# Optimization experiments

Hardware: AMD Instinct MI355X
Metric: run time of the kernel (lower is better)

## Reference

```python
import jax, jax.numpy as jnp
import numpy as np
from jax import lax

NUM_CODEBOOKS = 8
CODEBOOK_SIZE = 1024
HIDDEN_DIM = 512
NUM_LAYERS = 4
KSIZE = 15
COMMIT = 0.25


def _conv1d(x, w, b, stride, pad):
    # x: [B, Cin, L], w: [Cout, Cin, K] (torch Conv1d layout == OIH)
    y = lax.conv_general_dilated(x, w, window_strides=(stride,), padding=[(pad, pad)],
                                 dimension_numbers=('NCH', 'OIH', 'NCH'))
    return y + b[None, :, None]


def _conv_transpose1d(x, w, b):
    # torch ConvTranspose1d(k=15, stride=2, padding=7, output_padding=1)
    # w: [Cin, Cout, K] (torch layout). Equivalent fwd conv: flip kernel, swap io,
    # lhs_dilation=stride, padding=(K-1-pad, K-1-pad+output_padding) = (7, 8).
    wf = jnp.flip(w, -1).transpose(1, 0, 2)  # [Cout, Cin, K]
    y = lax.conv_general_dilated(x, wf, window_strides=(1,), padding=[(7, 8)],
                                 lhs_dilation=(2,), dimension_numbers=('NCH', 'OIH', 'NCH'))
    return y + b[None, :, None]


def _vq(residual, cb):
    # residual: [B, D, T], cb: [K, D]
    B, D, T = residual.shape
    z = residual.transpose(0, 2, 1).reshape(-1, D)  # [B*T, D]
    # ||z||^2 - 2 z C^T + ||C||^2
    dists = (z * z).sum(1, keepdims=True) - 2.0 * (z @ cb.T) + (cb * cb).sum(1)
    codes = jnp.argmin(dists, axis=1)  # [B*T]
    z_q = cb[codes].reshape(B, T, D).transpose(0, 2, 1)  # [B, D, T]
    commitment = jnp.mean((lax.stop_gradient(z_q) - residual) ** 2)
    codebook_l = jnp.mean((z_q - lax.stop_gradient(residual)) ** 2)
    vq_loss = codebook_l + COMMIT * commitment
    z_q_st = residual + lax.stop_gradient(z_q - residual)  # straight-through
    return z_q_st, vq_loss, codes.reshape(-1)


def _codec_forward(audio, enc_ws, enc_bs, codebooks, dec_ws, dec_bs):
    # encoder
    x = audio
    for w, b in zip(enc_ws, enc_bs):
        x = jax.nn.elu(_conv1d(x, w, b, stride=2, pad=7))
    z = x  # [B, 512, T]
    # residual VQ
    quantized = jnp.zeros_like(z)
    residual = z
    total_loss = jnp.float32(0.0)
    all_codes = []
    for i in range(NUM_CODEBOOKS):
        z_q, vq_loss, codes = _vq(residual, codebooks[i])
        quantized = quantized + z_q
        residual = residual - z_q
        total_loss = total_loss + vq_loss
        all_codes.append(codes)
    # decoder
    y = quantized
    for w, b in zip(dec_ws[:-1], dec_bs[:-1]):
        y = jax.nn.elu(_conv_transpose1d(y, w, b))
    y = jnp.tanh(_conv_transpose1d(y, dec_ws[-1], dec_bs[-1]))
    return y, total_loss, all_codes


def setup_inputs() -> dict:
    key = jax.random.key(0)
    ks = jax.random.split(key, 32)
    B, S = 8, 65536
    audio = jax.random.normal(ks[0], (B, 1, S), dtype=jnp.float32)
    # encoder channels: 1 -> 64 -> 128 -> 256 -> 512
    enc_ch = [1, 64, 128, 256, 512]
    inp = {'audio': audio}
    for i in range(NUM_LAYERS):
        cin, cout = enc_ch[i], enc_ch[i + 1]
        fan = cin * KSIZE
        inp[f'enc_w{i}'] = jax.random.normal(ks[1 + i], (cout, cin, KSIZE), jnp.float32) / np.sqrt(fan)
        inp[f'enc_b{i}'] = jnp.zeros((cout,), jnp.float32)
    # codebooks ~ U(-1/K, 1/K)
    inp['codebooks'] = jax.random.uniform(ks[10], (NUM_CODEBOOKS, CODEBOOK_SIZE, HIDDEN_DIM),
                                          jnp.float32, -1.0 / CODEBOOK_SIZE, 1.0 / CODEBOOK_SIZE)
    # decoder (torch ConvTranspose layout [Cin, Cout, K]): 512->256->128->64->1
    dec_ch = [512, 256, 128, 64, 1]
    for i in range(NUM_LAYERS):
        cin, cout = dec_ch[i], dec_ch[i + 1]
        fan = cin * KSIZE
        inp[f'dec_w{i}'] = jax.random.normal(ks[20 + i], (cin, cout, KSIZE), jnp.float32) / np.sqrt(fan)
        inp[f'dec_b{i}'] = jnp.zeros((cout,), jnp.float32)
    return inp


def reference(audio, enc_w0, enc_b0, enc_w1, enc_b1, enc_w2, enc_b2, enc_w3, enc_b3,
              codebooks, dec_w0, dec_b0, dec_w1, dec_b1, dec_w2, dec_b2, dec_w3, dec_b3):
    enc_ws = [enc_w0, enc_w1, enc_w2, enc_w3]
    enc_bs = [enc_b0, enc_b1, enc_b2, enc_b3]
    dec_ws = [dec_w0, dec_w1, dec_w2, dec_w3]
    dec_bs = [dec_b0, dec_b1, dec_b2, dec_b3]
    recon, vq_loss, codes = _codec_forward(audio, enc_ws, enc_bs, codebooks, dec_ws, dec_bs)
    return (recon, vq_loss, *codes)
```

## Files before the change

kernel.cpp:

```cpp
#include <hip/hip_runtime.h>
#include <hip/hip_bf16.h>
#include <math.h>

#define NCB 8
#define CBS 1024
#define HID 512
#define NB 8
#define TLAT 4096
#define DELTA 6.0e-5f

__global__ void rd_sentinel(float* out, float v)
{
    out[threadIdx.x] = v;
}

template<int CIN, int COUT, int LIN>
__global__ __launch_bounds__(256)
void rd_enc(const float* __restrict__ x, const float* __restrict__ w,
            const float* __restrict__ bias, float* __restrict__ y)
{
    constexpr int LOUT = LIN / 2;
    __shared__ float xs[2][528];
    const int tid = threadIdx.x;
    const int t0  = blockIdx.x * 512;
    const int t   = t0 + tid * 2;
    const int co0 = blockIdx.y * 4;
    const int b   = blockIdx.z;
    const float* xb = x + (size_t)b * CIN * LIN;
    const int base = 2 * t0 - 8;

    double acc[4][2];
#pragma unroll
    for (int c = 0; c < 4; ++c) acc[c][0] = acc[c][1] = (double)bias[co0 + c];

    for (int ci = 0; ci < CIN; ++ci) {
        const float* xc = xb + (size_t)ci * LIN;
        __syncthreads();
        for (int j = tid; j < 1040; j += 256) {
            const int xi = base + j;
            xs[j & 1][j >> 1] = ((unsigned)xi < (unsigned)LIN) ? xc[xi] : 0.f;
        }
        __syncthreads();
        const float* wc = w + ((size_t)co0 * CIN + ci) * 15;
#pragma unroll
        for (int k = 0; k < 15; ++k) {
            const int p = (k + 1) & 1;
            const int j = 2 * tid + ((k + 1) >> 1);
            const double x0 = (double)xs[p][j];
            const double x1 = (double)xs[p][j + 1];
#pragma unroll
            for (int c = 0; c < 4; ++c) {
                const double wv = (double)wc[c * CIN * 15 + k];
                acc[c][0] = fma(wv, x0, acc[c][0]);
                acc[c][1] = fma(wv, x1, acc[c][1]);
            }
        }
    }
#pragma unroll
    for (int c = 0; c < 4; ++c) {
        float* yp = y + ((size_t)b * COUT + co0 + c) * LOUT + t;
        const double a0 = acc[c][0], a1 = acc[c][1];
        yp[0] = (float)(a0 > 0.0 ? a0 : expm1(a0));
        yp[1] = (float)(a1 > 0.0 ? a1 : expm1(a1));
    }
}

template<int CIN, int COUT, int LIN, int CO_PER, int ACT>
__global__ __launch_bounds__(256)
void rd_dec(const float* __restrict__ x, const float* __restrict__ w,
            const float* __restrict__ bias, float* __restrict__ y)
{
    constexpr int LOUT = LIN * 2;
    const int u   = blockIdx.x * 256 + threadIdx.x;
    const int co0 = blockIdx.y * CO_PER;
    const int b   = blockIdx.z;

    float acc[CO_PER][2];
#pragma unroll
    for (int c = 0; c < CO_PER; ++c) acc[c][0] = acc[c][1] = bias[co0 + c];

    const float* xb = x + (size_t)b * CIN * LIN;
    for (int ci = 0; ci < CIN; ++ci) {
        const float* xc = xb + (size_t)ci * LIN;
        const float* wc = w + ((size_t)ci * COUT + co0) * 15;
#pragma unroll
        for (int dj = 0; dj < 8; ++dj) {
            const int j = u - 3 + dj;
            const float xv = ((unsigned)j < (unsigned)LIN) ? xc[j] : 0.f;
            const int ke = 13 - 2 * dj;
            const int ko = 14 - 2 * dj;
#pragma unroll
            for (int c = 0; c < CO_PER; ++c) {
                if (ke >= 0) acc[c][0] = fmaf(xv, wc[c * 15 + ke], acc[c][0]);
                acc[c][1] = fmaf(xv, wc[c * 15 + ko], acc[c][1]);
            }
        }
    }
#pragma unroll
    for (int c = 0; c < CO_PER; ++c) {
        float* yp = y + ((size_t)b * COUT + co0 + c) * LOUT + 2 * (size_t)u;
        if (ACT == 0) {
            yp[0] = acc[c][0] > 0.f ? acc[c][0] : expm1f(acc[c][0]);
            yp[1] = acc[c][1] > 0.f ? acc[c][1] : expm1f(acc[c][1]);
        } else {
            yp[0] = tanhf(acc[c][0]);
            yp[1] = tanhf(acc[c][1]);
        }
    }
}

__global__ __launch_bounds__(64)
void rd_prep(const float* __restrict__ cb, float* __restrict__ cnormF,
             float* __restrict__ lossp)
{
    __shared__ double red[64];
    const int rrow = blockIdx.x;
    const float* src = cb + (size_t)rrow * HID;
    const int lane = threadIdx.x;
    double s = 0.0;
#pragma unroll
    for (int m = 0; m < 8; ++m) {
        const float v = src[lane * 8 + m];
        s += (double)__fmul_rn(v, v);
    }
    red[lane] = s;
    __syncthreads();
    if (lane == 0) {
        double tot = 0.0;
        for (int i = 0; i < 64; ++i) tot += red[i];
        cnormF[rrow] = (float)tot;
        if (rrow == 0) lossp[0] = 0.f;
    }
}

__global__ __launch_bounds__(256)
void rd_z(const float* __restrict__ R, float* __restrict__ Zrow)
{
    __shared__ double zp[64][4];
    const int tid = threadIdx.x;
    const int gr0 = blockIdx.x * 64;
    const int b = gr0 >> 12, t0 = gr0 & 4095;
    const float* Rb = R + (size_t)b * HID * TLAT + t0;
    const int row = tid & 63, p = tid >> 6;
    double s = 0.0;
    const int d0 = p * 128;
    for (int d = d0; d < d0 + 128; ++d) {
        const float v = Rb[(size_t)d * TLAT + row];
        s += (double)__fmul_rn(v, v);
    }
    zp[row][p] = s;
    __syncthreads();
    if (tid < 64)
        Zrow[gr0 + tid] = (float)(((zp[tid][0] + zp[tid][1]) + zp[tid][2]) + zp[tid][3]);
}

__global__ __launch_bounds__(256)
void rd_pref(const float* __restrict__ cb, const float* __restrict__ cnormF,
             const float* __restrict__ R, float* __restrict__ tileMin)
{
    __shared__ __align__(16) float Rt[32][64];
    __shared__ __align__(16) float Ct[32][128];
    const int tid = threadIdx.x;
    const int gr0 = blockIdx.x * 64;
    const int cb0 = blockIdx.y * 128;
    const int b = gr0 >> 12, t0 = gr0 & 4095;
    const float* Rb = R + (size_t)b * HID * TLAT + t0;
    const int ir = tid >> 4, jc = tid & 15;

    float acc[4][8];
#pragma unroll
    for (int r = 0; r < 4; ++r)
#pragma unroll
        for (int c = 0; c < 8; ++c) acc[r][c] = 0.f;

    for (int kc = 0; kc < 16; ++kc) {
        const int k0 = kc * 32;
        __syncthreads();
#pragma unroll
        for (int l = 0; l < 8; ++l) {
            const int e = l * 256 + tid;
            Rt[e >> 6][e & 63] = Rb[(size_t)(k0 + (e >> 6)) * TLAT + (e & 63)];
        }
        {
            const int cc = tid >> 1, h = (tid & 1) * 16;
            const float* s = cb + (size_t)(cb0 + cc) * HID + k0 + h;
            const float4 v0 = *(const float4*)s;
            const float4 v1 = *(const float4*)(s + 4);
            const float4 v2 = *(const float4*)(s + 8);
            const float4 v3 = *(const float4*)(s + 12);
            Ct[h + 0][cc] = v0.x; Ct[h + 1][cc] = v0.y; Ct[h + 2][cc] = v0.z; Ct[h + 3][cc] = v0.w;
            Ct[h + 4][cc] = v1.x; Ct[h + 5][cc] = v1.y; Ct[h + 6][cc] = v1.z; Ct[h + 7][cc] = v1.w;
            Ct[h + 8][cc] = v2.x; Ct[h + 9][cc] = v2.y; Ct[h +10][cc] = v2.z; Ct[h +11][cc] = v2.w;
            Ct[h +12][cc] = v3.x; Ct[h +13][cc] = v3.y; Ct[h +14][cc] = v3.z; Ct[h +15][cc] = v3.w;
        }
        __syncthreads();

#pragma unroll
        for (int kk = 0; kk < 32; ++kk) {
            const float4 rv = *(const float4*)&Rt[kk][ir * 4];
            const float4 c0v = *(const float4*)&Ct[kk][jc * 8];
            const float4 c1v = *(const float4*)&Ct[kk][jc * 8 + 4];
            const float rr[4] = {rv.x, rv.y, rv.z, rv.w};
            const float cc8[8] = {c0v.x, c0v.y, c0v.z, c0v.w, c1v.x, c1v.y, c1v.z, c1v.w};
#pragma unroll
            for (int r = 0; r < 4; ++r)
#pragma unroll
                for (int c = 0; c < 8; ++c)
                    acc[r][c] = fmaf(rr[r], cc8[c], acc[r][c]);
        }
    }

#pragma unroll
    for (int r = 0; r < 4; ++r) {
        float m = 3.0e38f;
#pragma unroll
        for (int c = 0; c < 8; ++c) {
            const int ci = cb0 + jc * 8 + c;
            const float s = fmaf(-2.f, acc[r][c], cnormF[ci]);
            m = fminf(m, s);
        }
        const float o = __shfl_xor(m, 1, 64);
        m = fminf(m, o);
        if ((jc & 1) == 0)
            tileMin[(size_t)(gr0 + ir * 4 + r) * 64 + (cb0 >> 4) + (jc >> 1)] = m;
    }
}

__global__ __launch_bounds__(256)
void rd_fin(const float* __restrict__ cb, const float* __restrict__ cnormF,
            const float* __restrict__ R, const float* __restrict__ Zrow,
            const float* __restrict__ tileMin, unsigned short* __restrict__ codesOut)
{
    __shared__ float pm[64][4];
    __shared__ float rowMinS[64];
    __shared__ unsigned char tlist[64][16];
    __shared__ int tcnt[64];
    __shared__ int maxcS;
    __shared__ float bvS[64][4];
    __shared__ int   bcS[64][4];

    const int tid = threadIdx.x;
    const int gr0 = blockIdx.x * 64;
    const int b = gr0 >> 12, t0 = gr0 & 4095;
    const float* Rb = R + (size_t)b * HID * TLAT + t0;
    const int row = tid & 63, p = tid >> 6;
    const float* tmr = tileMin + (size_t)(gr0 + row) * 64;

    float m = 3.0e38f;
    for (int j = 0; j < 16; ++j) m = fminf(m, tmr[p * 16 + j]);
    pm[row][p] = m;
    if (tid == 0) maxcS = 0;
    __syncthreads();
    if (tid < 64)
        rowMinS[tid] = fminf(fminf(pm[tid][0], pm[tid][1]), fminf(pm[tid][2], pm[tid][3]));
    __syncthreads();

    if (tid < 64) {
        int cnt = 0;
        const float thr_ = rowMinS[tid] + DELTA;
        const float* tr = tileMin + (size_t)(gr0 + tid) * 64;
        for (int tt = 0; tt < 64; ++tt)
            if (tr[tt] <= thr_) { if (cnt < 16) tlist[tid][cnt] = (unsigned char)tt; ++cnt; }
        if (cnt > 16) cnt = 64;
        tcnt[tid] = cnt;
        atomicMax(&maxcS, cnt);
    }
    __syncthreads();
    const int maxc = maxcS;
    const int myCnt = tcnt[row];
    const float Zr = Zrow[gr0 + row];

    float bestS = 3.0e38f; int bestC = 0x7fffffff;
    for (int li = 0; li < maxc; ++li) {
        int tt = -1;
        if (li < myCnt) tt = (myCnt <= 16) ? (int)tlist[row][li] : li;
        if (tt >= 0) {
            const float* cp = cb + (size_t)(tt * 16 + p * 4) * HID;
            double a0 = 0.0, a1 = 0.0, a2 = 0.0, a3 = 0.0;
            for (int d = 0; d < 512; ++d) {
                const double rv = (double)Rb[(size_t)d * TLAT + row];
                a0 = fma(rv, (double)cp[d],        a0);
                a1 = fma(rv, (double)cp[d + 512],  a1);
                a2 = fma(rv, (double)cp[d + 1024], a2);
                a3 = fma(rv, (double)cp[d + 1536], a3);
            }
            const double aa[4] = {a0, a1, a2, a3};
#pragma unroll
            for (int c = 0; c < 4; ++c) {
                const int ci = tt * 16 + p * 4 + c;
                const float M32 = (float)aa[c];
                const float s = __fadd_rn(__fsub_rn(Zr, __fadd_rn(M32, M32)), cnormF[ci]);
                if (s < bestS || (s == bestS && ci < bestC)) { bestS = s; bestC = ci; }
            }
        }
    }
    bvS[row][p] = bestS; bcS[row][p] = bestC;
    __syncthreads();
    if (tid < 64) {
        float mv = 3.0e38f; int mc = 0x7fffffff;
#pragma unroll
        for (int q = 0; q < 4; ++q) {
            const float v = bvS[tid][q]; const int c = bcS[tid][q];
            if (v < mv || (v == mv && c < mc)) { mv = v; mc = c; }
        }
        codesOut[gr0 + tid] = (unsigned short)mc;
    }
}

__global__ __launch_bounds__(256)
void rd_comb(const float* __restrict__ cb, const unsigned short* __restrict__ codesIn,
             float* __restrict__ R, float* __restrict__ Q,
             float* __restrict__ loss_acc, int stage)
{
    __shared__ int codes_l[64];
    const int tid = threadIdx.x;
    const int gr0 = blockIdx.x * 64;
    const int b = gr0 >> 12, t0 = gr0 & 4095;
    float* Rb = R + (size_t)b * HID * TLAT + t0;
    float* Qb = Q + (size_t)b * HID * TLAT + t0;

    if (tid < 64) codes_l[tid] = (int)codesIn[gr0 + tid];
    __syncthreads();

    float ls = 0.f;
    for (int e = tid; e < 64 * HID; e += 256) {
        const int row = e & 63, d = e >> 6;
        const size_t off = (size_t)d * TLAT + row;
        const float rr = Rb[off];
        const int c = codes_l[row];
        const float q = cb[(size_t)c * HID + d];
        const float diff  = __fsub_rn(q, rr);
        const float zqst  = __fadd_rn(rr, diff);
        ls = fmaf(diff, diff, ls);
        Rb[off] = __fsub_rn(rr, zqst);
        if (stage == 0) Qb[off] = zqst; else Qb[off] = __fadd_rn(Qb[off], zqst);
    }
#pragma unroll
    for (int off = 32; off; off >>= 1) ls += __shfl_down(ls, off, 64);
    if ((tid & 63) == 0) atomicAdd(loss_acc, ls);
}

__global__ __launch_bounds__(256)
void rd_emit(const float* __restrict__ reconF, const unsigned short* __restrict__ codes_ws,
             const float* __restrict__ loss_acc, float* __restrict__ out)
{
    const int j = blockIdx.x * 256 + threadIdx.x;
    if (j >= 524288 + 1 + NCB * 32768) return;
    if (j < 524288)       out[j] = reconF[j];
    else if (j == 524288) out[j] = loss_acc[0] * 1.25f * (1.0f / 16777216.0f);
    else                  out[j] = (float)codes_ws[j - 524289];
}

extern "C" void kernel_launch(void* const* d_in, const int* in_sizes, int n_in,
                              void* d_out, int out_size, void* d_ws, size_t ws_size,
                              hipStream_t stream)
{
    float* out = (float*)d_out;

    if (n_in != 18)                                   { rd_sentinel<<<1, 256, 0, stream>>>(out, 1111.0f); return; }
    if (in_sizes[0] != 8 * 65536 || in_sizes[9] != NCB * CBS * HID ||
        in_sizes[1] != 64 * 15 || in_sizes[10] != 512 * 256 * 15)
                                                      { rd_sentinel<<<1, 256, 0, stream>>>(out, 3333.0f); return; }
    if (out_size != 524288 + 1 + NCB * 32768)         { rd_sentinel<<<1, 256, 0, stream>>>(out, 5555.0f); return; }
    if (ws_size < (size_t)137 * 1024 * 1024)          { rd_sentinel<<<1, 256, 0, stream>>>(out, 7777.0f); return; }

    const float* audio = (const float*)d_in[0];
    const float *ew[4], *eb[4], *dw[4], *db[4];
    for (int i = 0; i < 4; ++i) { ew[i] = (const float*)d_in[1 + 2 * i]; eb[i] = (const float*)d_in[2 + 2 * i]; }
    const float* cbs = (const float*)d_in[9];
    for (int i = 0; i < 4; ++i) { dw[i] = (const float*)d_in[10 + 2 * i]; db[i] = (const float*)d_in[11 + 2 * i]; }

    char* ws = (char*)d_ws;
    float*  A        = (float*)ws;
    float*  Bb       = (float*)(ws + (size_t)64 * 1024 * 1024);
    float*  tileMin  = (float*)(ws + (size_t)128 * 1024 * 1024);
    float*  reconF   = (float*)(ws + (size_t)128 * 1024 * 1024);
    unsigned short* codes_ws = (unsigned short*)(ws + (size_t)136 * 1024 * 1024);
    float*  cnormF   = (float*)(ws + (size_t)136 * 1024 * 1024 + 524288);
    float*  Zrow     = (float*)(ws + (size_t)136 * 1024 * 1024 + 524288 + 32768);
    float*  lossp    = (float*)(ws + (size_t)136 * 1024 * 1024 + 524288 + 32768 + 131072);

    rd_prep<<<NCB * CBS, 64, 0, stream>>>(cbs, cnormF, lossp);

    rd_enc<1,   64,  65536><<<dim3(64, 16,  NB), 256, 0, stream>>>(audio, ew[0], eb[0], A);
    rd_enc<64,  128, 32768><<<dim3(32, 32,  NB), 256, 0, stream>>>(A,  ew[1], eb[1], Bb);
    rd_enc<128, 256, 16384><<<dim3(16, 64,  NB), 256, 0, stream>>>(Bb, ew[2], eb[2], A);
    rd_enc<256, 512, 8192 ><<<dim3(8,  128, NB), 256, 0, stream>>>(A,  ew[3], eb[3], Bb);

    for (int i = 0; i < NCB; ++i) {
        const float* cbi = cbs + (size_t)i * CBS * HID;
        const float* cni = cnormF + (size_t)i * CBS;
        rd_z   <<<512, 256, 0, stream>>>(Bb, Zrow);
        rd_pref<<<dim3(512, 8), 256, 0, stream>>>(cbi, cni, Bb, tileMin);
        rd_fin <<<512, 256, 0, stream>>>(cbi, cni, Bb, Zrow, tileMin,
                                         codes_ws + (size_t)i * 32768);
        rd_comb<<<512, 256, 0, stream>>>(cbi, codes_ws + (size_t)i * 32768,
                                         Bb, A, lossp, i);
    }

    rd_dec<512, 256, 4096,  4, 0><<<dim3(16,  64, NB), 256, 0, stream>>>(A,  dw[0], db[0], Bb);
    rd_dec<256, 128, 8192,  4, 0><<<dim3(32,  32, NB), 256, 0, stream>>>(Bb, dw[1], db[1], A);
    rd_dec<128, 64,  16384, 4, 0><<<dim3(64,  16, NB), 256, 0, stream>>>(A,  dw[2], db[2], Bb);
    rd_dec<64,  1,   32768, 1, 1><<<dim3(128, 1,  NB), 256, 0, stream>>>(Bb, dw[3], db[3], reconF);

    rd_emit<<<3073, 256, 0, stream>>>(reconF, codes_ws, lossp, out);
}
```

Before: 18.58 ms.

## Transpose latent to row-major for VQ stage and remap encoder output pairs

Adds a tiled transpose kernel that converts the encoder output from [B, D, T] to [B*T, D] before the residual VQ loop and back afterwards. The VQ kernels (norms, distance tiles, refinement, combine) now read and write contiguous rows with vectorised float4 loads instead of strided column accesses. The encoder conv also changes each thread's two outputs from adjacent to 256 apart, giving coalesced stores and conflict-free LDS reads. The cost is two extra full-tensor transposes.

New measurement: 19.08 ms. +2.7%, slower.

```diff
diff --git a/kernel.cpp b/kernel.cpp
--- a/kernel.cpp
+++ b/kernel.cpp
@@ -9,21 +9,20 @@
 #define TLAT 4096
 #define DELTA 6.0e-5f
 
-__global__ void rd_sentinel(float* out, float v)
+__global__ void re_sentinel(float* out, float v)
 {
     out[threadIdx.x] = v;
 }
 
 template<int CIN, int COUT, int LIN>
 __global__ __launch_bounds__(256)
-void rd_enc(const float* __restrict__ x, const float* __restrict__ w,
+void re_enc(const float* __restrict__ x, const float* __restrict__ w,
             const float* __restrict__ bias, float* __restrict__ y)
 {
     constexpr int LOUT = LIN / 2;
-    __shared__ float xs[2][528];
+    __shared__ float xs[2][520];
     const int tid = threadIdx.x;
     const int t0  = blockIdx.x * 512;
-    const int t   = t0 + tid * 2;
     const int co0 = blockIdx.y * 4;
     const int b   = blockIdx.z;
     const float* xb = x + (size_t)b * CIN * LIN;
@@ -36,18 +35,18 @@
     for (int ci = 0; ci < CIN; ++ci) {
         const float* xc = xb + (size_t)ci * LIN;
         __syncthreads();
-        for (int j = tid; j < 1040; j += 256) {
-            const int xi = base + j;
-            xs[j & 1][j >> 1] = ((unsigned)xi < (unsigned)LIN) ? xc[xi] : 0.f;
+        for (int idx = tid; idx < 1040; idx += 256) {
+            const int xi = base + idx;
+            xs[idx & 1][idx >> 1] = ((unsigned)xi < (unsigned)LIN) ? xc[xi] : 0.f;
         }
         __syncthreads();
         const float* wc = w + ((size_t)co0 * CIN + ci) * 15;
 #pragma unroll
         for (int k = 0; k < 15; ++k) {
-            const int p = (k + 1) & 1;
-            const int j = 2 * tid + ((k + 1) >> 1);
-            const double x0 = (double)xs[p][j];
-            const double x1 = (double)xs[p][j + 1];
+            const int p  = (k + 1) & 1;
+            const int jb = (k + 1) >> 1;
+            const double x0 = (double)xs[p][tid + jb];
+            const double x1 = (double)xs[p][tid + 256 + jb];
 #pragma unroll
             for (int c = 0; c < 4; ++c) {
                 const double wv = (double)wc[c * CIN * 15 + k];
@@ -58,16 +57,34 @@
     }
 #pragma unroll
     for (int c = 0; c < 4; ++c) {
-        float* yp = y + ((size_t)b * COUT + co0 + c) * LOUT + t;
+        float* yp = y + ((size_t)b * COUT + co0 + c) * LOUT;
         const double a0 = acc[c][0], a1 = acc[c][1];
-        yp[0] = (float)(a0 > 0.0 ? a0 : expm1(a0));
-        yp[1] = (float)(a1 > 0.0 ? a1 : expm1(a1));
-    }
+        yp[t0 + tid]       = (float)(a0 > 0.0 ? a0 : expm1(a0));
+        yp[t0 + tid + 256] = (float)(a1 > 0.0 ? a1 : expm1(a1));
+    }
+}
+
+template<int RIN, int CIN_>
+__global__ __launch_bounds__(256)
+void re_tr(const float* __restrict__ in, float* __restrict__ out)
+{
+    __shared__ float tile[32][33];
+    const int c0 = blockIdx.x * 32, r0 = blockIdx.y * 32, b = blockIdx.z;
+    const int lx = threadIdx.x & 31, ly = threadIdx.x >> 5;
+    const float* ib = in + (size_t)b * RIN * CIN_;
+    float* ob = out + (size_t)b * RIN * CIN_;
+#pragma unroll
+    for (int m = 0; m < 4; ++m)
+        tile[ly + m * 8][lx] = ib[(size_t)(r0 + ly + m * 8) * CIN_ + c0 + lx];
+    __syncthreads();
+#pragma unroll
+    for (int m = 0; m < 4; ++m)
+        ob[(size_t)(c0 + ly + m * 8) * RIN + r0 + lx] = tile[lx][ly + m * 8];
 }
 
 template<int CIN, int COUT, int LIN, int CO_PER, int ACT>
 __global__ __launch_bounds__(256)
-void rd_dec(const float* __restrict__ x, const float* __restrict__ w,
+void re_dec(const float* __restrict__ x, const float* __restrict__ w,
             const float* __restrict__ bias, float* __restrict__ y)
 {
     constexpr int LOUT = LIN * 2;
@@ -110,7 +127,7 @@
 }
 
 __global__ __launch_bounds__(64)
-void rd_prep(const float* __restrict__ cb, float* __restrict__ cnormF,
+void re_prep(const float* __restrict__ cb, float* __restrict__ cnormF,
              float* __restrict__ lossp)
 {
     __shared__ double red[64];
@@ -134,18 +151,16 @@
 }
 
 __global__ __launch_bounds__(256)
-void rd_z(const float* __restrict__ R, float* __restrict__ Zrow)
+void re_z(const float* __restrict__ R, float* __restrict__ Zrow)
 {
     __shared__ double zp[64][4];
     const int tid = threadIdx.x;
     const int gr0 = blockIdx.x * 64;
-    const int b = gr0 >> 12, t0 = gr0 & 4095;
-    const float* Rb = R + (size_t)b * HID * TLAT + t0;
     const int row = tid & 63, p = tid >> 6;
+    const float* Rr = R + (size_t)(gr0 + row) * HID + p * 128;
     double s = 0.0;
-    const int d0 = p * 128;
-    for (int d = d0; d < d0 + 128; ++d) {
-        const float v = Rb[(size_t)d * TLAT + row];
+    for (int i = 0; i < 128; ++i) {
+        const float v = Rr[i];
         s += (double)__fmul_rn(v, v);
     }
     zp[row][p] = s;
@@ -155,7 +170,7 @@
 }
 
 __global__ __launch_bounds__(256)
-void rd_pref(const float* __restrict__ cb, const float* __restrict__ cnormF,
+void re_pref(const float* __restrict__ cb, const float* __restrict__ cnormF,
              const float* __restrict__ R, float* __restrict__ tileMin)
 {
     __shared__ __align__(16) float Rt[32][64];
@@ -163,8 +178,7 @@
     const int tid = threadIdx.x;
     const int gr0 = blockIdx.x * 64;
     const int cb0 = blockIdx.y * 128;
-    const int b = gr0 >> 12, t0 = gr0 & 4095;
-    const float* Rb = R + (size_t)b * HID * TLAT + t0;
+    const float* Rbase = R + (size_t)gr0 * HID;
     const int ir = tid >> 4, jc = tid & 15;
 
     float acc[4][8];
@@ -177,9 +191,12 @@
         const int k0 = kc * 32;
         __syncthreads();
 #pragma unroll
-        for (int l = 0; l < 8; ++l) {
-            const int e = l * 256 + tid;
-            Rt[e >> 6][e & 63] = Rb[(size_t)(k0 + (e >> 6)) * TLAT + (e & 63)];
+        for (int rep = 0; rep < 2; ++rep) {
+            const int row  = (tid >> 3) + 32 * rep;
+            const int koff = (tid & 7) * 4;
+            const float4 v = *(const float4*)(Rbase + (size_t)row * HID + k0 + koff);
+            Rt[koff + 0][row] = v.x; Rt[koff + 1][row] = v.y;
+            Rt[koff + 2][row] = v.z; Rt[koff + 3][row] = v.w;
         }
         {
             const int cc = tid >> 1, h = (tid & 1) * 16;
@@ -227,7 +244,7 @@
 }
 
 __global__ __launch_bounds__(256)
-void rd_fin(const float* __restrict__ cb, const float* __restrict__ cnormF,
+void re_fin(const float* __restrict__ cb, const float* __restrict__ cnormF,
             const float* __restrict__ R, const float* __restrict__ Zrow,
             const float* __restrict__ tileMin, unsigned short* __restrict__ codesOut)
 {
@@ -241,9 +258,8 @@
 
     const int tid = threadIdx.x;
     const int gr0 = blockIdx.x * 64;
-    const int b = gr0 >> 12, t0 = gr0 & 4095;
-    const float* Rb = R + (size_t)b * HID * TLAT + t0;
     const int row = tid & 63, p = tid >> 6;
+    const float* Rr = R + (size_t)(gr0 + row) * HID;
     const float* tmr = tileMin + (size_t)(gr0 + row) * 64;
 
     float m = 3.0e38f;
@@ -278,7 +294,7 @@
             const float* cp = cb + (size_t)(tt * 16 + p * 4) * HID;
             double a0 = 0.0, a1 = 0.0, a2 = 0.0, a3 = 0.0;
             for (int d = 0; d < 512; ++d) {
-                const double rv = (double)Rb[(size_t)d * TLAT + row];
+                const double rv = (double)Rr[d];
                 a0 = fma(rv, (double)cp[d],        a0);
                 a1 = fma(rv, (double)cp[d + 512],  a1);
                 a2 = fma(rv, (double)cp[d + 1024], a2);
@@ -308,32 +324,30 @@
 }
 
 __global__ __launch_bounds__(256)
-void rd_comb(const float* __restrict__ cb, const unsigned short* __restrict__ codesIn,
+void re_comb(const float* __restrict__ cb, const unsigned short* __restrict__ codesIn,
              float* __restrict__ R, float* __restrict__ Q,
              float* __restrict__ loss_acc, int stage)
 {
     __shared__ int codes_l[64];
     const int tid = threadIdx.x;
     const int gr0 = blockIdx.x * 64;
-    const int b = gr0 >> 12, t0 = gr0 & 4095;
-    float* Rb = R + (size_t)b * HID * TLAT + t0;
-    float* Qb = Q + (size_t)b * HID * TLAT + t0;
+    float* Rb = R + (size_t)gr0 * HID;
+    float* Qb = Q + (size_t)gr0 * HID;
 
     if (tid < 64) codes_l[tid] = (int)codesIn[gr0 + tid];
     __syncthreads();
 
     float ls = 0.f;
     for (int e = tid; e < 64 * HID; e += 256) {
-        const int row = e & 63, d = e >> 6;
-        const size_t off = (size_t)d * TLAT + row;
-        const float rr = Rb[off];
+        const int row = e >> 9;
         const int c = codes_l[row];
-        const float q = cb[(size_t)c * HID + d];
+        const float rr = Rb[e];
+        const float q = cb[(size_t)c * HID + (e & 511)];
         const float diff  = __fsub_rn(q, rr);
         const float zqst  = __fadd_rn(rr, diff);
         ls = fmaf(diff, diff, ls);
-        Rb[off] = __fsub_rn(rr, zqst);
-        if (stage == 0) Qb[off] = zqst; else Qb[off] = __fadd_rn(Qb[off], zqst);
+        Rb[e] = __fsub_rn(rr, zqst);
+        if (stage == 0) Qb[e] = zqst; else Qb[e] = __fadd_rn(Qb[e], zqst);
     }
 #pragma unroll
     for (int off = 32; off; off >>= 1) ls += __shfl_down(ls, off, 64);
@@ -341,7 +355,7 @@
 }
 
 __global__ __launch_bounds__(256)
-void rd_emit(const float* __restrict__ reconF, const unsigned short* __restrict__ codes_ws,
+void re_emit(const float* __restrict__ reconF, const unsigned short* __restrict__ codes_ws,
              const float* __restrict__ loss_acc, float* __restrict__ out)
 {
     const int j = blockIdx.x * 256 + threadIdx.x;
@@ -357,12 +371,12 @@
 {
     float* out = (float*)d_out;
 
-    if (n_in != 18)                                   { rd_sentinel<<<1, 256, 0, stream>>>(out, 1111.0f); return; }
+    if (n_in != 18)                                   { re_sentinel<<<1, 256, 0, stream>>>(out, 1111.0f); return; }
     if (in_sizes[0] != 8 * 65536 || in_sizes[9] != NCB * CBS * HID ||
         in_sizes[1] != 64 * 15 || in_sizes[10] != 512 * 256 * 15)
-                                                      { rd_sentinel<<<1, 256, 0, stream>>>(out, 3333.0f); return; }
-    if (out_size != 524288 + 1 + NCB * 32768)         { rd_sentinel<<<1, 256, 0, stream>>>(out, 5555.0f); return; }
-    if (ws_size < (size_t)137 * 1024 * 1024)          { rd_sentinel<<<1, 256, 0, stream>>>(out, 7777.0f); return; }
+                                                      { re_sentinel<<<1, 256, 0, stream>>>(out, 3333.0f); return; }
+    if (out_size != 524288 + 1 + NCB * 32768)         { re_sentinel<<<1, 256, 0, stream>>>(out, 5555.0f); return; }
+    if (ws_size < (size_t)137 * 1024 * 1024)          { re_sentinel<<<1, 256, 0, stream>>>(out, 7777.0f); return; }
 
     const float* audio = (const float*)d_in[0];
     const float *ew[4], *eb[4], *dw[4], *db[4];
@@ -380,28 +394,32 @@
     float*  Zrow     = (float*)(ws + (size_t)136 * 1024 * 1024 + 524288 + 32768);
     float*  lossp    = (float*)(ws + (size_t)136 * 1024 * 1024 + 524288 + 32768 + 131072);
 
-    rd_prep<<<NCB * CBS, 64, 0, stream>>>(cbs, cnormF, lossp);
-
-    rd_enc<1,   64,  65536><<<dim3(64, 16,  NB), 256, 0, stream>>>(audio, ew[0], eb[0], A);
-    rd_enc<64,  128, 32768><<<dim3(32, 32,  NB), 256, 0, stream>>>(A,  ew[1], eb[1], Bb);
-    rd_enc<128, 256, 16384><<<dim3(16, 64,  NB), 256, 0, stream>>>(Bb, ew[2], eb[2], A);
-    rd_enc<256, 512, 8192 ><<<dim3(8,  128, NB), 256, 0, stream>>>(A,  ew[3], eb[3], Bb);
+    re_prep<<<NCB * CBS, 64, 0, stream>>>(cbs, cnormF, lossp);
+
+    re_enc<1,   64,  65536><<<dim3(64, 16,  NB), 256, 0, stream>>>(audio, ew[0], eb[0], A);
+    re_enc<64,  128, 32768><<<dim3(32, 32,  NB), 256, 0, stream>>>(A,  ew[1], eb[1], Bb);
+    re_enc<128, 256, 16384><<<dim3(16, 64,  NB), 256, 0, stream>>>(Bb, ew[2], eb[2], A);
+    re_enc<256, 512, 8192 ><<<dim3(8,  128, NB), 256, 0, stream>>>(A,  ew[3], eb[3], Bb);
+
+    re_tr<512, 4096><<<dim3(128, 16, NB), 256, 0, stream>>>(Bb, A);
 
     for (int i = 0; i < NCB; ++i) {
         const float* cbi = cbs + (size_t)i * CBS * HID;
         const float* cni = cnormF + (size_t)i * CBS;
-        rd_z   <<<512, 256, 0, stream>>>(Bb, Zrow);
-        rd_pref<<<dim3(512, 8), 256, 0, stream>>>(cbi, cni, Bb, tileMin);
-        rd_fin <<<512, 256, 0, stream>>>(cbi, cni, Bb, Zrow, tileMin,
+        re_z   <<<512, 256, 0, stream>>>(A, Zrow);
+        re_pref<<<dim3(512, 8), 256, 0, stream>>>(cbi, cni, A, tileMin);
+        re_fin <<<512, 256, 0, stream>>>(cbi, cni, A, Zrow, tileMin,
                                          codes_ws + (size_t)i * 32768);
-        rd_comb<<<512, 256, 0, stream>>>(cbi, codes_ws + (size_t)i * 32768,
-                                         Bb, A, lossp, i);
-    }
-
-    rd_dec<512, 256, 4096,  4, 0><<<dim3(16,  64, NB), 256, 0, stream>>>(A,  dw[0], db[0], Bb);
-    rd_dec<256, 128, 8192,  4, 0><<<dim3(32,  32, NB), 256, 0, stream>>>(Bb, dw[1], db[1], A);
-    rd_dec<128, 64,  16384, 4, 0><<<dim3(64,  16, NB), 256, 0, stream>>>(A,  dw[2], db[2], Bb);
-    rd_dec<64,  1,   32768, 1, 1><<<dim3(128, 1,  NB), 256, 0, stream>>>(Bb, dw[3], db[3], reconF);
-
-    rd_emit<<<3073, 256, 0, stream>>>(reconF, codes_ws, lossp, out);
-}
+        re_comb<<<512, 256, 0, stream>>>(cbi, codes_ws + (size_t)i * 32768,
+                                         A, Bb, lossp, i);
+    }
+
+    re_tr<4096, 512><<<dim3(16, 128, NB), 256, 0, stream>>>(Bb, A);
+
+    re_dec<512, 256, 4096,  4, 0><<<dim3(16,  64, NB), 256, 0, stream>>>(A,  dw[0], db[0], Bb);
+    re_dec<256, 128, 8192,  4, 0><<<dim3(32,  32, NB), 256, 0, stream>>>(Bb, dw[1], db[1], A);
+    re_dec<128, 64,  16384, 4, 0><<<dim3(64,  16, NB), 256, 0, stream>>>(A,  dw[2], db[2], Bb);
+    re_dec<64,  1,   32768, 1, 1><<<dim3(128, 1,  NB), 256, 0, stream>>>(Bb, dw[3], db[3], reconF);
+
+    re_emit<<<3073, 256, 0, stream>>>(reconF, codes_ws, lossp, out);
+}
```
